# Kernel tuning notes

Hardware: AMD Instinct MI355X
Metric: run time of the kernel (lower is better)

Reference implementation:

```python
import jax, jax.numpy as jnp
import numpy as np

NUM_HEADS = 32
NUM_KV_HEADS = 8
HEAD_DIM = 64
ROPE_THETA = 10000.0


def setup_inputs() -> dict:
    key = jax.random.key(0)
    ks = jax.random.split(key, 5)
    B, N, D = 2, 2048, 2048
    kv_out = NUM_KV_HEADS * HEAD_DIM
    s = 0.02
    return {
        "x": jax.random.normal(ks[0], (B, N, D), dtype=jnp.float32),
        "Wq": jax.random.normal(ks[1], (D, D), dtype=jnp.float32) * s,
        "Wk": jax.random.normal(ks[2], (kv_out, D), dtype=jnp.float32) * s,
        "Wv": jax.random.normal(ks[3], (kv_out, D), dtype=jnp.float32) * s,
        "Wo": jax.random.normal(ks[4], (D, D), dtype=jnp.float32) * s,
    }


def _rotate_half(t):
    d = t.shape[-1] // 2
    return jnp.concatenate([-t[..., d:], t[..., :d]], axis=-1)


def _rope_cos_sin(N, dtype):
    # Llama rotary embedding: inv_freq over even dims, duplicated along last axis
    inv_freq = 1.0 / (ROPE_THETA ** (jnp.arange(0, HEAD_DIM, 2, dtype=jnp.float32) / HEAD_DIM))
    freqs = jnp.arange(N, dtype=jnp.float32)[:, None] * inv_freq[None, :]  # [N, hd/2]
    emb = jnp.concatenate([freqs, freqs], axis=-1)  # [N, hd]
    return jnp.cos(emb).astype(dtype), jnp.sin(emb).astype(dtype)


def reference(x, Wq, Wk, Wv, Wo):
    B, N, D = x.shape
    groups = NUM_HEADS // NUM_KV_HEADS
    scale = HEAD_DIM ** -0.5

    q = (x @ Wq.T).reshape(B, N, NUM_HEADS, HEAD_DIM).transpose(0, 2, 1, 3)      # [B,H,N,hd]
    k = (x @ Wk.T).reshape(B, N, NUM_KV_HEADS, HEAD_DIM).transpose(0, 2, 1, 3)   # [B,KVH,N,hd]
    v = (x @ Wv.T).reshape(B, N, NUM_KV_HEADS, HEAD_DIM).transpose(0, 2, 1, 3)

    cos, sin = _rope_cos_sin(N, x.dtype)  # [N,hd]
    cos = cos[None, None]  # [1,1,N,hd]
    sin = sin[None, None]
    q = q * cos + _rotate_half(q) * sin
    k = k * cos + _rotate_half(k) * sin

    # repeat_kv: [B,KVH,N,hd] -> [B,H,N,hd]
    k = jnp.repeat(k, groups, axis=1)
    v = jnp.repeat(v, groups, axis=1)

    attn = jnp.einsum('bhqd,bhkd->bhqk', q, k) * scale  # [B,H,N,N]
    attn = jax.nn.softmax(attn, axis=-1)
    out = jnp.einsum('bhqk,bhkd->bhqd', attn, v)        # [B,H,N,hd]
    out = out.transpose(0, 2, 1, 3).reshape(B, N, D)
    return out @ Wo.T
```

## Files before the change

### kernel.cpp

```cpp
#include <hip/hip_runtime.h>
#include <hip/hip_bf16.h>

#define Bc 2
#define Nc 2048
#define Dc 2048
#define Hc 32
#define KVHc 8

typedef __attribute__((ext_vector_type(4))) float f32x4;
typedef __attribute__((ext_vector_type(8))) short short8;

__device__ __forceinline__ ushort f2b(float f) {
  union { float f; unsigned u; } v; v.f = f;
  unsigned u = v.u;
  unsigned r = (u + 0x7FFFu + ((u >> 16) & 1u)) >> 16;
  return (ushort)r;
}
__device__ __forceinline__ float b2f(ushort h) {
  union { unsigned u; float f; } v; v.u = ((unsigned)h) << 16; return v.f;
}

__device__ __forceinline__ float fexp2(float x) {
  float r;
  asm("v_exp_f32 %0, %1" : "=v"(r) : "v"(x));
  return r;
}

__device__ __forceinline__ unsigned cvt_pk_bf16(float lo, float hi) {
  unsigned r;
  asm("v_cvt_pk_bf16_f32 %0, %1, %2" : "=v"(r) : "v"(lo), "v"(hi));
  return r;
}

__device__ __forceinline__ void gload_lds16(const ushort* g, ushort* l) {
  __builtin_amdgcn_global_load_lds(
      (const __attribute__((address_space(1))) void*)g,
      (__attribute__((address_space(3))) void*)l, 16, 0, 0);
}

template<int ITERS>
__device__ __forceinline__ void stage_tile(const ushort* gbase, int gstride,
                                           ushort* lds, int tid) {
  #pragma unroll
  for (int i = 0; i < ITERS; ++i) {
    int s = i * 256 + tid;
    int row = s >> 3;
    int sch = (s & 7) ^ (row & 7);
    gload_lds16(gbase + (size_t)row * gstride + sch * 8, lds + s * 8);
  }
}
__device__ __forceinline__ short8 read_frag(const ushort* lds, int row, int kbyte) {
  int off = kbyte ^ ((row & 7) << 4);
  return *(const short8*)((const char*)lds + row * 128 + off);
}

__device__ __forceinline__ int f_attn(int row) {
  return ((row >> 1) & 1) | (((row >> 3) & 1) << 1) |
         ((((row >> 2) ^ (row >> 4)) & 1) << 2);
}

__global__ void k_convert_all(
    const float* __restrict__ x,  const float* __restrict__ wq,
    const float* __restrict__ wk, const float* __restrict__ wv,
    const float* __restrict__ wo, ushort* __restrict__ xb,
    ushort* __restrict__ wqkv, ushort* __restrict__ wob) {
  int i = blockIdx.x * 256 + threadIdx.x;
  const float* src; ushort* dst; int off;
  if (i < 2097152)      { src = x;  dst = xb;             off = i; }
  else if (i < 3145728) { src = wq; dst = wqkv;           off = i - 2097152; }
  else if (i < 3407872) { src = wk; dst = wqkv + 4194304; off = i - 3145728; }
  else if (i < 3670016) { src = wv; dst = wqkv + 5242880; off = i - 3407872; }
  else                  { src = wo; dst = wob;            off = i - 3670016; }
  float4 v = ((const float4*)src)[off];
  ushort4 o;
  o.x = f2b(v.x); o.y = f2b(v.y); o.z = f2b(v.z); o.w = f2b(v.w);
  *(ushort4*)&dst[(size_t)off * 4] = o;
}

__global__ void k_rope_table(float* __restrict__ cosT, float* __restrict__ sinT) {
  int i = blockIdx.x * 256 + threadIdx.x;
  int n = i >> 5, f = i & 31;
  float inv = powf(10000.0f, -(float)f * (1.0f / 32.0f));
  float ang = (float)n * inv;
  cosT[i] = cosf(ang);
  sinT[i] = sinf(ang);
}

__global__ __launch_bounds__(512, 2) void k_gemm8(
    const ushort* __restrict__ A, const ushort* __restrict__ Bm,
    ushort* __restrict__ C, int M, int Nn, int K) {
  __shared__ ushort lds[2][2][2][128 * 64];
  int nt = Nn >> 8;
  int bid0 = blockIdx.x;
  int bid = (bid0 & 7) * ((int)gridDim.x >> 3) + (bid0 >> 3);
  int m0 = (bid / nt) << 8, n0 = (bid % nt) << 8;
  int tid = threadIdx.x;
  int lane = tid & 63, w = tid >> 6;
  int wr = w >> 2, wc = w & 3;
  int lc = lane & 15, lq = lane >> 4;
  int nkt = K >> 6, nit = nkt >> 1;

  const ushort* Ag = A + (size_t)m0 * K;
  const ushort* Bg = Bm + (size_t)n0 * K;

  int r0s = tid >> 3;
  int sch = (tid & 7) ^ (r0s & 7);
  size_t g0 = (size_t)r0s * K + sch * 8;
  size_t g1 = (size_t)(64 + r0s) * K + sch * 8;
  int l0 = tid * 8, l1 = 4096 + tid * 8;

  int sw = (lc & 7) << 4;
  int koff0 = (lq * 16) ^ sw;
  int koff1 = (64 + lq * 16) ^ sw;
  int abase = lc * 128;
  int bbase = ((wc & 1) * 64 + lc) * 128;

  f32x4 acc[8][4];
  #pragma unroll
  for (int r = 0; r < 8; ++r)
    #pragma unroll
    for (int c = 0; c < 4; ++c) acc[r][c] = (f32x4){0.f, 0.f, 0.f, 0.f};
  short8 afr[4][2], bfr[4][2];

  auto STAGE = [&](int op, int h, int t) {
    if (t >= nkt) t -= nkt;
    const ushort* gb = (op ? Bg : Ag) + (size_t)(h * 128) * K + t * 64;
    ushort* lb = &lds[t & 1][op][h][0];
    gload_lds16(gb + g0, lb + l0);
    gload_lds16(gb + g1, lb + l1);
  };
  auto LDA = [&](int b, int mh) {
    const char* p = (const char*)&lds[b][0][wr][0];
    #pragma unroll
    for (int mi = 0; mi < 4; ++mi) {
      int rb = abase + (mh * 4 + mi) * 2048;
      afr[mi][0] = *(const short8*)(p + rb + koff0);
      afr[mi][1] = *(const short8*)(p + rb + koff1);
    }
  };
  auto LDB = [&](int b, int nh) {
    const char* p = (const char*)&lds[b][1][wc >> 1][0];
    #pragma unroll
    for (int ni = 0; ni < 2; ++ni) {
      int rb = bbase + (nh * 2 + ni) * 2048;
      bfr[nh * 2 + ni][0] = *(const short8*)(p + rb + koff0);
      bfr[nh * 2 + ni][1] = *(const short8*)(p + rb + koff1);
    }
  };
  auto MFMA16 = [&](int mh, int nh) {
    __builtin_amdgcn_s_setprio(1);
    #pragma unroll
    for (int mi = 0; mi < 4; ++mi)
      #pragma unroll
      for (int ni = 0; ni < 2; ++ni) {
        f32x4 a = acc[mh * 4 + mi][nh * 2 + ni];
        a = __builtin_amdgcn_mfma_f32_16x16x32_bf16(afr[mi][0], bfr[nh * 2 + ni][0], a, 0, 0, 0);
        a = __builtin_amdgcn_mfma_f32_16x16x32_bf16(afr[mi][1], bfr[nh * 2 + ni][1], a, 0, 0, 0);
        acc[mh * 4 + mi][nh * 2 + ni] = a;
      }
    __builtin_amdgcn_s_setprio(0);
  };

  #define BAR __builtin_amdgcn_s_barrier()
  #define LGK do { asm volatile("s_waitcnt lgkmcnt(0)" ::: "memory"); \
                   __builtin_amdgcn_sched_barrier(0); } while (0)
  #define VM4 asm volatile("s_waitcnt vmcnt(4)" ::: "memory")

  STAGE(1, 0, 0); STAGE(0, 0, 0); STAGE(0, 1, 0); STAGE(1, 1, 0);
  STAGE(1, 0, 1); STAGE(1, 1, 1);
  VM4; BAR;

  for (int i = 0; i < nit; ++i) {
    int t1 = 2 * i + 1;
    LDA(0, 0); LDB(0, 0); STAGE(0, 0, t1);
    BAR; LGK; MFMA16(0, 0); BAR;
    LDB(0, 1); STAGE(0, 1, t1);
    BAR; LGK; MFMA16(0, 1); BAR;
    LDA(0, 1); STAGE(1, 0, t1 + 1);
    BAR; LGK; MFMA16(1, 1); BAR;
    STAGE(0, 0, t1 + 1);
    BAR; MFMA16(1, 0); VM4; BAR;
    LDA(1, 0); LDB(1, 0); STAGE(0, 1, t1 + 1);
    BAR; LGK; MFMA16(0, 0); BAR;
    LDB(1, 1); STAGE(1, 1, t1 + 1);
    BAR; LGK; MFMA16(0, 1); BAR;
    LDA(1, 1); STAGE(1, 0, t1 + 2);
    BAR; LGK; MFMA16(1, 1); BAR;
    STAGE(1, 1, t1 + 2);
    BAR; MFMA16(1, 0); VM4; BAR;
  }
  #undef BAR
  #undef LGK
  #undef VM4

  #pragma unroll
  for (int mf = 0; mf < 8; ++mf)
    #pragma unroll
    for (int nf = 0; nf < 4; ++nf) {
      int gr = m0 + wr * 128 + mf * 16 + lq * 4;
      int gc = n0 + wc * 64 + nf * 16 + lc;
      #pragma unroll
      for (int e = 0; e < 4; ++e)
        C[(size_t)(gr + e) * Nn + gc] = f2b(acc[mf][nf][e]);
    }
}

template<typename TOUT>
__global__ __launch_bounds__(256) void k_gemm_bt(
    const ushort* __restrict__ A, const ushort* __restrict__ Bm,
    TOUT* __restrict__ C, int M, int Nn, int K) {
  __shared__ ushort ldsA[128 * 64];
  __shared__ ushort ldsB[128 * 64];
  int nt = Nn >> 7;
  int bid0 = blockIdx.x;
  int bid = (bid0 & 7) * ((int)gridDim.x >> 3) + (bid0 >> 3);
  int m0 = (bid / nt) << 7;
  int n0 = (bid % nt) << 7;
  int tid = threadIdx.x;
  int lane = tid & 63, w = tid >> 6;
  int wr = w >> 1, wc = w & 1;
  int lc = lane & 15, lq = lane >> 4;
  f32x4 acc[4][4];
  #pragma unroll
  for (int r = 0; r < 4; ++r)
    #pragma unroll
    for (int c = 0; c < 4; ++c) acc[r][c] = (f32x4){0.f, 0.f, 0.f, 0.f};
  int nkt = K >> 6;
  for (int kt = 0; kt < nkt; ++kt) {
    stage_tile<4>(A + (size_t)m0 * K + kt * 64, K, ldsA, tid);
    stage_tile<4>(Bm + (size_t)n0 * K + kt * 64, K, ldsB, tid);
    __syncthreads();
    #pragma unroll
    for (int kk = 0; kk < 2; ++kk) {
      int kbyte = kk * 64 + lq * 16;
      short8 af[4], bfr[4];
      #pragma unroll
      for (int r = 0; r < 4; ++r) af[r] = read_frag(ldsA, wr * 64 + r * 16 + lc, kbyte);
      #pragma unroll
      for (int c = 0; c < 4; ++c) bfr[c] = read_frag(ldsB, wc * 64 + c * 16 + lc, kbyte);
      #pragma unroll
      for (int r = 0; r < 4; ++r)
        #pragma unroll
        for (int c = 0; c < 4; ++c)
          acc[r][c] = __builtin_amdgcn_mfma_f32_16x16x32_bf16(af[r], bfr[c], acc[r][c], 0, 0, 0);
    }
    __syncthreads();
  }
  #pragma unroll
  for (int r = 0; r < 4; ++r)
    #pragma unroll
    for (int c = 0; c < 4; ++c) {
      int gr = m0 + wr * 64 + r * 16 + lq * 4;
      int gc = n0 + wc * 64 + c * 16 + lc;
      #pragma unroll
      for (int e = 0; e < 4; ++e) {
        float val = acc[r][c][e];
        if constexpr (sizeof(TOUT) == 2)
          C[(size_t)(gr + e) * Nn + gc] = f2b(val);
        else
          C[(size_t)(gr + e) * Nn + gc] = val;
      }
    }
}

__global__ void k_rope_qk(const ushort* __restrict__ qkv,
                          const float* __restrict__ cosT, const float* __restrict__ sinT,
                          ushort* __restrict__ qr, ushort* __restrict__ kr) {
  const float QS = 0.125f * 1.44269504089f;
  int bn = blockIdx.x;
  int b = bn >> 11, n = bn & (Nc - 1);
  int t = threadIdx.x;
  const ushort* row = qkv + (size_t)bn * 3072;
  #pragma unroll
  for (int i = 0; i < 4; ++i) {
    int p = i * 256 + t;
    int h = p >> 5, dp = p & 31;
    float c = cosT[n * 32 + dp], s = sinT[n * 32 + dp];
    float q0 = b2f(row[h * 64 + dp]);
    float q1 = b2f(row[h * 64 + dp + 32]);
    size_t ob = ((size_t)(b * Hc + h) * Nc + n) * 64 + dp;
    qr[ob]      = f2b((q0 * c - q1 * s) * QS);
    qr[ob + 32] = f2b((q1 * c + q0 * s) * QS);
  }
  {
    int kvh = t >> 5, dp = t & 31;
    float c = cosT[n * 32 + dp], s = sinT[n * 32 + dp];
    float k0 = b2f(row[2048 + kvh * 64 + dp]);
    float k1 = b2f(row[2048 + kvh * 64 + dp + 32]);
    size_t ob = ((size_t)(b * KVHc + kvh) * Nc + n) * 64 + dp;
    kr[ob]      = f2b(k0 * c - k1 * s);
    kr[ob + 32] = f2b(k1 * c + k0 * s);
  }
}

__global__ void k_transpose_v(const ushort* __restrict__ qkv, ushort* __restrict__ vt) {
  __shared__ ushort tile[64][72];
  int bid = blockIdx.x;
  int ntile = bid & 31, kvh = (bid >> 5) & 7, b = bid >> 8;
  int t = threadIdx.x;
  int n0 = ntile * 64;
  #pragma unroll
  for (int i = 0; i < 4; ++i) {
    int s = i * 256 + t;
    int r = s >> 4, c4 = s & 15;
    ushort4 v = *(const ushort4*)&qkv[(size_t)(b * Nc + n0 + r) * 3072 + 2560 + kvh * 64 + c4 * 4];
    tile[r][c4 * 4 + 0] = v.x; tile[r][c4 * 4 + 1] = v.y;
    tile[r][c4 * 4 + 2] = v.z; tile[r][c4 * 4 + 3] = v.w;
  }
  __syncthreads();
  #pragma unroll
  for (int i = 0; i < 4; ++i) {
    int s = i * 256 + t;
    int d = s >> 4, c4 = s & 15;
    ushort4 v;
    v.x = tile[c4 * 4 + 0][d]; v.y = tile[c4 * 4 + 1][d];
    v.z = tile[c4 * 4 + 2][d]; v.w = tile[c4 * 4 + 3][d];
    *(ushort4*)&vt[(size_t)((b * KVHc + kvh) * 64 + d) * Nc + n0 + c4 * 4] = v;
  }
}

__global__ __launch_bounds__(512) void k_attn(
    const ushort* __restrict__ qr, const ushort* __restrict__ kr,
    const ushort* __restrict__ vt, ushort* __restrict__ ctx) {
  __shared__ ushort ldsK[2][2][64 * 64];
  __shared__ ushort ldsV[2][2][64 * 64];
  int bid = blockIdx.x;
  int qt = bid & 31, p = (bid >> 5) & 1, kvh = (bid >> 6) & 7, b = bid >> 9;
  int tid = threadIdx.x;
  int w = tid >> 6, lane = tid & 63;
  int lc = lane & 15, lq = lane >> 4;
  int h = kvh * 4 + p * 2 + (w >> 2);
  int q0 = qt * 64 + (w & 3) * 16;
  const ushort* Qb = qr + (size_t)(b * Hc + h) * Nc * 64;
  const ushort* Kb = kr + (size_t)(b * KVHc + kvh) * Nc * 64;
  const ushort* Vb = vt + (size_t)(b * KVHc + kvh) * 64 * Nc;
  short8 aq[2];
  #pragma unroll
  for (int kk = 0; kk < 2; ++kk)
    aq[kk] = *(const short8*)&Qb[(size_t)(q0 + lc) * 64 + kk * 32 + lq * 8];

  int offK[2][4], offV[2][4];
  #pragma unroll
  for (int c = 0; c < 4; ++c) {
    int rowK = ((c >> 1) << 5) + ((lc >> 2) << 3) + ((c & 1) << 2) + (lc & 3);
    int fs = f_attn(rowK) << 4;
    #pragma unroll
    for (int kk = 0; kk < 2; ++kk)
      offK[kk][c] = rowK * 128 + ((kk * 64 + lq * 16) ^ fs);
  }
  #pragma unroll
  for (int dd = 0; dd < 4; ++dd) {
    int rowV = dd * 16 + lc;
    int fs = f_attn(rowV) << 4;
    #pragma unroll
    for (int kk = 0; kk < 2; ++kk)
      offV[kk][dd] = rowV * 128 + ((kk * 64 + lq * 16) ^ fs);
  }

  int r0 = tid >> 3;
  int c0 = (tid & 7) ^ f_attn(r0);
  int oK0 = r0 * 64 + c0 * 8;
  int oK1 = (64 + r0) * 64 + c0 * 8;
  int oV0 = r0 * Nc + c0 * 8;
  int oV1 = r0 * Nc + 64 + c0 * 8;
  int d0 = tid * 8;

  f32x4 oacc[4];
  #pragma unroll
  for (int d = 0; d < 4; ++d) oacc[d] = (f32x4){0.f, 0.f, 0.f, 0.f};
  float lpart = 0.f;

  auto compute = [&](const ushort* lK, const ushort* lV) {
    f32x4 sc[4];
    __builtin_amdgcn_s_setprio(1);
    #pragma unroll
    for (int c = 0; c < 4; ++c) {
      f32x4 a = (f32x4){0.f, 0.f, 0.f, 0.f};
      #pragma unroll
      for (int kk = 0; kk < 2; ++kk)
        a = __builtin_amdgcn_mfma_f32_16x16x32_bf16(
            *(const short8*)((const char*)lK + offK[kk][c]), aq[kk], a, 0, 0, 0);
      sc[c] = a;
    }
    __builtin_amdgcn_s_setprio(0);
    float ps[4];
    #pragma unroll
    for (int c = 0; c < 4; ++c) {
      #pragma unroll
      for (int e = 0; e < 4; ++e)
        sc[c][e] = fexp2(sc[c][e]);
      ps[c] = (sc[c][0] + sc[c][1]) + (sc[c][2] + sc[c][3]);
    }
    lpart += (ps[0] + ps[1]) + (ps[2] + ps[3]);
    unsigned pk[4][2];
    #pragma unroll
    for (int c = 0; c < 4; ++c) {
      pk[c][0] = cvt_pk_bf16(sc[c][0], sc[c][1]);
      pk[c][1] = cvt_pk_bf16(sc[c][2], sc[c][3]);
    }
    __builtin_amdgcn_s_setprio(1);
    #pragma unroll
    for (int kk = 0; kk < 2; ++kk) {
      union { short8 s; unsigned u[4]; } pa;
      pa.u[0] = pk[2 * kk][0];
      pa.u[1] = pk[2 * kk][1];
      pa.u[2] = pk[2 * kk + 1][0];
      pa.u[3] = pk[2 * kk + 1][1];
      #pragma unroll
      for (int dd = 0; dd < 4; ++dd)
        oacc[dd] = __builtin_amdgcn_mfma_f32_16x16x32_bf16(
            *(const short8*)((const char*)lV + offV[kk][dd]), pa.s, oacc[dd], 0, 0, 0);
    }
    __builtin_amdgcn_s_setprio(0);
  };

  auto stage128 = [&](int buf) {
    gload_lds16(Kb + oK0, &ldsK[buf][0][d0]);
    gload_lds16(Kb + oK1, &ldsK[buf][1][d0 - 4096 >= 0 ? d0 - 4096 + 4096 : d0]);
    gload_lds16(Vb + oV0, &ldsV[buf][0][d0]);
    gload_lds16(Vb + oV1, &ldsV[buf][1][d0]);
  };
  (void)stage128;

  gload_lds16(Kb + oK0, &ldsK[0][0][d0]);
  gload_lds16(Kb + oK1, &ldsK[0][1][d0]);
  gload_lds16(Vb + oV0, &ldsV[0][0][d0]);
  gload_lds16(Vb + oV1, &ldsV[0][1][d0]);
  oK0 += 8192; oK1 += 8192; oV0 += 128; oV1 += 128;
  __syncthreads();

  constexpr int NT2 = Nc / 128;
  for (int t2 = 0; t2 < NT2; t2 += 2) {
    gload_lds16(Kb + oK0, &ldsK[1][0][d0]);
    gload_lds16(Kb + oK1, &ldsK[1][1][d0]);
    gload_lds16(Vb + oV0, &ldsV[1][0][d0]);
    gload_lds16(Vb + oV1, &ldsV[1][1][d0]);
    oK0 += 8192; oK1 += 8192; oV0 += 128; oV1 += 128;
    compute(&ldsK[0][0][0], &ldsV[0][0][0]);
    compute(&ldsK[0][1][0], &ldsV[0][1][0]);
    __syncthreads();
    if (t2 + 2 < NT2) {
      gload_lds16(Kb + oK0, &ldsK[0][0][d0]);
      gload_lds16(Kb + oK1, &ldsK[0][1][d0]);
      gload_lds16(Vb + oV0, &ldsV[0][0][d0]);
      gload_lds16(Vb + oV1, &ldsV[0][1][d0]);
    }
    oK0 += 8192; oK1 += 8192; oV0 += 128; oV1 += 128;
    compute(&ldsK[1][0][0], &ldsV[1][0][0]);
    compute(&ldsK[1][1][0], &ldsV[1][1][0]);
    __syncthreads();
  }
  float lrun = lpart;
  lrun += __shfl_xor(lrun, 16, 64);
  lrun += __shfl_xor(lrun, 32, 64);
  float rinv = 1.f / lrun;
  #pragma unroll
  for (int dd = 0; dd < 4; ++dd) {
    ushort4 o;
    o.x = f2b(oacc[dd][0] * rinv);
    o.y = f2b(oacc[dd][1] * rinv);
    o.z = f2b(oacc[dd][2] * rinv);
    o.w = f2b(oacc[dd][3] * rinv);
    *(ushort4*)&ctx[(size_t)(b * Nc + q0 + lc) * Dc + h * 64 + dd * 16 + lq * 4] = o;
  }
}

extern "C" void kernel_launch(void* const* d_in, const int* in_sizes, int n_in,
                              void* d_out, int out_size, void* d_ws, size_t ws_size,
                              hipStream_t stream) {
  const float* x  = (const float*)d_in[0];
  const float* Wq = (const float*)d_in[1];
  const float* Wk = (const float*)d_in[2];
  const float* Wv = (const float*)d_in[3];
  const float* Wo = (const float*)d_in[4];

  ushort* ws   = (ushort*)d_ws;
  ushort* xb   = ws;
  ushort* wqkv = xb + 8388608;
  ushort* wob  = wqkv + 6291456;
  float*  cosT = (float*)(wob + 4194304);
  float*  sinT = cosT + 65536;
  ushort* qkv  = (ushort*)(sinT + 65536);
  ushort* qr   = qkv + 12582912;
  ushort* kr   = qr + 8388608;
  ushort* vt   = kr + 2097152;
  ushort* ctx  = vt + 2097152;

  k_convert_all<<<18432, 256, 0, stream>>>(x, Wq, Wk, Wv, Wo, xb, wqkv, wob);
  k_rope_table<<<256, 256, 0, stream>>>(cosT, sinT);

  k_gemm8<<<192, 512, 0, stream>>>(xb, wqkv, qkv, 4096, 3072, 2048);
  k_rope_qk<<<4096, 256, 0, stream>>>(qkv, cosT, sinT, qr, kr);
  k_transpose_v<<<512, 256, 0, stream>>>(qkv, vt);
  k_attn<<<1024, 512, 0, stream>>>(qr, kr, vt, ctx);
  k_gemm_bt<float><<<512, 256, 0, stream>>>(ctx, wob, (float*)d_out, 4096, 2048, 2048);
}
```

Baseline: 206.6 us.

## Process two query tiles per wave in attention to reuse K/V LDS fragments

Each attention block now covers 128 query rows instead of 64, with every wave holding two 16-row query fragments. Each K and V fragment read from LDS feeds two MFMAs, which halves LDS reads and global K/V staging per query row. The grid halves to 512 blocks, which lowers parallelism on a many-CU GPU, and the doubled accumulators and score registers raise register pressure.

```diff
diff --git a/kernel.cpp b/kernel.cpp
--- a/kernel.cpp
+++ b/kernel.cpp
@@ -325,19 +325,21 @@
   __shared__ ushort ldsK[2][2][64 * 64];
   __shared__ ushort ldsV[2][2][64 * 64];
   int bid = blockIdx.x;
-  int qt = bid & 31, p = (bid >> 5) & 1, kvh = (bid >> 6) & 7, b = bid >> 9;
+  int qt = bid & 15, p = (bid >> 4) & 1, kvh = (bid >> 5) & 7, b = bid >> 8;
   int tid = threadIdx.x;
   int w = tid >> 6, lane = tid & 63;
   int lc = lane & 15, lq = lane >> 4;
   int h = kvh * 4 + p * 2 + (w >> 2);
-  int q0 = qt * 64 + (w & 3) * 16;
+  int q0 = qt * 128 + (w & 3) * 16;
   const ushort* Qb = qr + (size_t)(b * Hc + h) * Nc * 64;
   const ushort* Kb = kr + (size_t)(b * KVHc + kvh) * Nc * 64;
   const ushort* Vb = vt + (size_t)(b * KVHc + kvh) * 64 * Nc;
-  short8 aq[2];
-  #pragma unroll
-  for (int kk = 0; kk < 2; ++kk)
-    aq[kk] = *(const short8*)&Qb[(size_t)(q0 + lc) * 64 + kk * 32 + lq * 8];
+  short8 aqA[2], aqB[2];
+  #pragma unroll
+  for (int kk = 0; kk < 2; ++kk) {
+    aqA[kk] = *(const short8*)&Qb[(size_t)(q0 + lc) * 64 + kk * 32 + lq * 8];
+    aqB[kk] = *(const short8*)&Qb[(size_t)(q0 + 64 + lc) * 64 + kk * 32 + lq * 8];
+  }
 
   int offK[2][4], offV[2][4];
   #pragma unroll
@@ -365,62 +367,61 @@
   int oV1 = r0 * Nc + 64 + c0 * 8;
   int d0 = tid * 8;
 
-  f32x4 oacc[4];
-  #pragma unroll
-  for (int d = 0; d < 4; ++d) oacc[d] = (f32x4){0.f, 0.f, 0.f, 0.f};
-  float lpart = 0.f;
+  f32x4 oaccA[4], oaccB[4];
+  #pragma unroll
+  for (int d = 0; d < 4; ++d) {
+    oaccA[d] = (f32x4){0.f, 0.f, 0.f, 0.f};
+    oaccB[d] = (f32x4){0.f, 0.f, 0.f, 0.f};
+  }
+  float lpA = 0.f, lpB = 0.f;
 
   auto compute = [&](const ushort* lK, const ushort* lV) {
-    f32x4 sc[4];
+    f32x4 scA[4], scB[4];
     __builtin_amdgcn_s_setprio(1);
     #pragma unroll
     for (int c = 0; c < 4; ++c) {
+      short8 kf0 = *(const short8*)((const char*)lK + offK[0][c]);
+      short8 kf1 = *(const short8*)((const char*)lK + offK[1][c]);
       f32x4 a = (f32x4){0.f, 0.f, 0.f, 0.f};
-      #pragma unroll
-      for (int kk = 0; kk < 2; ++kk)
-        a = __builtin_amdgcn_mfma_f32_16x16x32_bf16(
-            *(const short8*)((const char*)lK + offK[kk][c]), aq[kk], a, 0, 0, 0);
-      sc[c] = a;
+      a = __builtin_amdgcn_mfma_f32_16x16x32_bf16(kf0, aqA[0], a, 0, 0, 0);
+      scA[c] = __builtin_amdgcn_mfma_f32_16x16x32_bf16(kf1, aqA[1], a, 0, 0, 0);
+      f32x4 bacc = (f32x4){0.f, 0.f, 0.f, 0.f};
+      bacc = __builtin_amdgcn_mfma_f32_16x16x32_bf16(kf0, aqB[0], bacc, 0, 0, 0);
+      scB[c] = __builtin_amdgcn_mfma_f32_16x16x32_bf16(kf1, aqB[1], bacc, 0, 0, 0);
     }
     __builtin_amdgcn_s_setprio(0);
-    float ps[4];
+    unsigned pkA[4][2], pkB[4][2];
     #pragma unroll
     for (int c = 0; c < 4; ++c) {
       #pragma unroll
-      for (int e = 0; e < 4; ++e)
-        sc[c][e] = fexp2(sc[c][e]);
-      ps[c] = (sc[c][0] + sc[c][1]) + (sc[c][2] + sc[c][3]);
-    }
-    lpart += (ps[0] + ps[1]) + (ps[2] + ps[3]);
-    unsigned pk[4][2];
-    #pragma unroll
-    for (int c = 0; c < 4; ++c) {
-      pk[c][0] = cvt_pk_bf16(sc[c][0], sc[c][1]);
-      pk[c][1] = cvt_pk_bf16(sc[c][2], sc[c][3]);
+      for (int e = 0; e < 4; ++e) {
+        scA[c][e] = fexp2(scA[c][e]);
+        scB[c][e] = fexp2(scB[c][e]);
+      }
+      lpA += (scA[c][0] + scA[c][1]) + (scA[c][2] + scA[c][3]);
+      lpB += (scB[c][0] + scB[c][1]) + (scB[c][2] + scB[c][3]);
+      pkA[c][0] = cvt_pk_bf16(scA[c][0], scA[c][1]);
+      pkA[c][1] = cvt_pk_bf16(scA[c][2], scA[c][3]);
+      pkB[c][0] = cvt_pk_bf16(scB[c][0], scB[c][1]);
+      pkB[c][1] = cvt_pk_bf16(scB[c][2], scB[c][3]);
     }
     __builtin_amdgcn_s_setprio(1);
     #pragma unroll
     for (int kk = 0; kk < 2; ++kk) {
-      union { short8 s; unsigned u[4]; } pa;
-      pa.u[0] = pk[2 * kk][0];
-      pa.u[1] = pk[2 * kk][1];
-      pa.u[2] = pk[2 * kk + 1][0];
-      pa.u[3] = pk[2 * kk + 1][1];
-      #pragma unroll
-      for (int dd = 0; dd < 4; ++dd)
-        oacc[dd] = __builtin_amdgcn_mfma_f32_16x16x32_bf16(
-            *(const short8*)((const char*)lV + offV[kk][dd]), pa.s, oacc[dd], 0, 0, 0);
+      union { short8 s; unsigned u[4]; } paA, paB;
+      paA.u[0] = pkA[2 * kk][0]; paA.u[1] = pkA[2 * kk][1];
+      paA.u[2] = pkA[2 * kk + 1][0]; paA.u[3] = pkA[2 * kk + 1][1];
+      paB.u[0] = pkB[2 * kk][0]; paB.u[1] = pkB[2 * kk][1];
+      paB.u[2] = pkB[2 * kk + 1][0]; paB.u[3] = pkB[2 * kk + 1][1];
+      #pragma unroll
+      for (int dd = 0; dd < 4; ++dd) {
+        short8 vf = *(const short8*)((const char*)lV + offV[kk][dd]);
+        oaccA[dd] = __builtin_amdgcn_mfma_f32_16x16x32_bf16(vf, paA.s, oaccA[dd], 0, 0, 0);
+        oaccB[dd] = __builtin_amdgcn_mfma_f32_16x16x32_bf16(vf, paB.s, oaccB[dd], 0, 0, 0);
+      }
     }
     __builtin_amdgcn_s_setprio(0);
   };
-
-  auto stage128 = [&](int buf) {
-    gload_lds16(Kb + oK0, &ldsK[buf][0][d0]);
-    gload_lds16(Kb + oK1, &ldsK[buf][1][d0 - 4096 >= 0 ? d0 - 4096 + 4096 : d0]);
-    gload_lds16(Vb + oV0, &ldsV[buf][0][d0]);
-    gload_lds16(Vb + oV1, &ldsV[buf][1][d0]);
-  };
-  (void)stage128;
 
   gload_lds16(Kb + oK0, &ldsK[0][0][d0]);
   gload_lds16(Kb + oK1, &ldsK[0][1][d0]);
@@ -450,18 +451,21 @@
     compute(&ldsK[1][1][0], &ldsV[1][1][0]);
     __syncthreads();
   }
-  float lrun = lpart;
-  lrun += __shfl_xor(lrun, 16, 64);
-  lrun += __shfl_xor(lrun, 32, 64);
-  float rinv = 1.f / lrun;
+  float lrA = lpA, lrB = lpB;
+  lrA += __shfl_xor(lrA, 16, 64);
+  lrA += __shfl_xor(lrA, 32, 64);
+  lrB += __shfl_xor(lrB, 16, 64);
+  lrB += __shfl_xor(lrB, 32, 64);
+  float riA = 1.f / lrA, riB = 1.f / lrB;
   #pragma unroll
   for (int dd = 0; dd < 4; ++dd) {
-    ushort4 o;
-    o.x = f2b(oacc[dd][0] * rinv);
-    o.y = f2b(oacc[dd][1] * rinv);
-    o.z = f2b(oacc[dd][2] * rinv);
-    o.w = f2b(oacc[dd][3] * rinv);
-    *(ushort4*)&ctx[(size_t)(b * Nc + q0 + lc) * Dc + h * 64 + dd * 16 + lq * 4] = o;
+    ushort4 oA, oB;
+    oA.x = f2b(oaccA[dd][0] * riA); oA.y = f2b(oaccA[dd][1] * riA);
+    oA.z = f2b(oaccA[dd][2] * riA); oA.w = f2b(oaccA[dd][3] * riA);
+    oB.x = f2b(oaccB[dd][0] * riB); oB.y = f2b(oaccB[dd][1] * riB);
+    oB.z = f2b(oaccB[dd][2] * riB); oB.w = f2b(oaccB[dd][3] * riB);
+    *(ushort4*)&ctx[(size_t)(b * Nc + q0 + lc) * Dc + h * 64 + dd * 16 + lq * 4] = oA;
+    *(ushort4*)&ctx[(size_t)(b * Nc + q0 + 64 + lc) * Dc + h * 64 + dd * 16 + lq * 4] = oB;
   }
 }
 
@@ -492,6 +496,6 @@
   k_gemm8<<<192, 512, 0, stream>>>(xb, wqkv, qkv, 4096, 3072, 2048);
   k_rope_qk<<<4096, 256, 0, stream>>>(qkv, cosT, sinT, qr, kr);
   k_transpose_v<<<512, 256, 0, stream>>>(qkv, vt);
-  k_attn<<<1024, 512, 0, stream>>>(qr, kr, vt, ctx);
+  k_attn<<<512, 512, 0, stream>>>(qr, kr, vt, ctx);
   k_gemm_bt<float><<<512, 256, 0, stream>>>(ctx, wob, (float*)d_out, 4096, 2048, 2048);
 }
```

Result: faster. 198.8 us (-3.8%).
